# Performance work log

Hardware: AMD Instinct MI355X
Metric: run time of the kernel (lower is better)

The kernel has to match this reference:

```python
import jax, jax.numpy as jnp
import numpy as np

EMBED = 2048
HEADS = 16
NOPE = 128      # embed // heads
VDIM = 128
ROPE = 64
Q_HEAD = NOPE + ROPE  # 192
KV_RANK = 512
BASE = 10000.0


def _rope(x, offset=0):
    # x: [b, h, n, d] with d even; rotary (lrpe_type=1) on pair-interleaved dims
    d = x.shape[-1]
    n = x.shape[-2]
    theta = BASE ** (-2.0 * jnp.arange(d // 2, dtype=jnp.float32) / d)  # [d/2]
    pos = jnp.arange(n, dtype=jnp.float32) + offset                     # [n]
    ang = pos[:, None] * theta[None, :]                                  # [n, d/2]
    cos, sin = jnp.cos(ang), jnp.sin(ang)
    x1 = x[..., 0::2]
    x2 = x[..., 1::2]
    o1 = x1 * cos - x2 * sin
    o2 = x1 * sin + x2 * cos
    return jnp.stack([o1, o2], axis=-1).reshape(x.shape)


def setup_inputs() -> dict:
    key = jax.random.key(0)
    ks = jax.random.split(key, 6)
    b, n = 2, 2048
    s = lambda fin: 1.0 / np.sqrt(fin)
    return {
        "x": jax.random.normal(ks[0], (b, n, EMBED), jnp.float32),
        "Wqa": jax.random.normal(ks[1], (EMBED, 512), jnp.float32) * s(EMBED),
        "Wqb": jax.random.normal(ks[2], (512, HEADS * Q_HEAD), jnp.float32) * s(512),
        "Wkva": jax.random.normal(ks[3], (EMBED, KV_RANK + ROPE), jnp.float32) * s(EMBED),
        "Wkvb": jax.random.normal(ks[4], (KV_RANK, HEADS * (NOPE + VDIM)), jnp.float32) * s(KV_RANK),
        "Wout": jax.random.normal(ks[5], (HEADS * VDIM, EMBED), jnp.float32) * s(HEADS * VDIM),
    }


def reference(x, Wqa, Wqb, Wkva, Wkvb, Wout):
    b, n, _ = x.shape
    # low-rank Q projection
    q = (x @ Wqa) @ Wqb                                   # [b, n, h*192]
    q = q.reshape(b, n, HEADS, Q_HEAD).transpose(0, 2, 1, 3)  # [b, h, n, 192]
    q_nope, q_pe = q[..., :NOPE], q[..., NOPE:]
    # low-rank KV compression + shared rope key
    ckv = x @ Wkva                                        # [b, n, 512+64]
    compressed, k_pe = ckv[..., :KV_RANK], ckv[..., KV_RANK:]
    k_pe = jnp.broadcast_to(k_pe[:, None], (b, HEADS, n, ROPE))
    kv = compressed @ Wkvb                                # [b, n, h*(128+128)]
    kv = kv.reshape(b, n, HEADS, NOPE + VDIM).transpose(0, 2, 1, 3)
    k_nope, v = kv[..., :NOPE], kv[..., NOPE:]
    # partial RoPE on rope slice
    q_pe = _rope(q_pe)
    k_pe = _rope(k_pe)
    qf = jnp.concatenate([q_nope, q_pe], axis=-1)         # [b, h, n, 192]
    kf = jnp.concatenate([k_nope, k_pe], axis=-1)
    # causal SDPA, scale = 1/sqrt(q_head_dim)
    scale = 1.0 / np.sqrt(Q_HEAD)
    scores = jnp.einsum("bhnd,bhmd->bhnm", qf, kf) * scale
    causal = jnp.tril(jnp.ones((n, n), dtype=bool))
    scores = jnp.where(causal, scores, jnp.finfo(scores.dtype).min)
    attn = jax.nn.softmax(scores, axis=-1)
    out = jnp.einsum("bhnm,bhmd->bhnd", attn, v)          # [b, h, n, 128]
    out = out.transpose(0, 2, 1, 3).reshape(b, n, HEADS * VDIM)
    return out @ Wout
```

## Files before the change

### kernel.cpp

```cpp
#include <hip/hip_runtime.h>
#include <math.h>

typedef __bf16 bf16;
typedef __bf16 bf16x8 __attribute__((ext_vector_type(8)));
typedef float f32x4 __attribute__((ext_vector_type(4)));

#define HEADS 16
#define QHEAD 192
#define NB 2
#define SEQ 2048
#define ROWS (NB * SEQ)
#define QSCALE2 0.10411754584f
#define CSHIFT 11.5415603272f

__global__ __launch_bounds__(256) void prep(
    const float* __restrict__ x,
    const float* __restrict__ Wqa, const float* __restrict__ Wqb,
    const float* __restrict__ Wkva, const float* __restrict__ Wkvb,
    const float* __restrict__ Wout,
    bf16* __restrict__ xb,
    bf16* __restrict__ WfT, bf16* __restrict__ WqbT,
    bf16* __restrict__ WkvbT, bf16* __restrict__ WoutT)
{
    int t = blockIdx.x;
    if (t < 8192) {
        size_t i = ((size_t)t * 256 + threadIdx.x) * 4;
        float4 v = *(const float4*)(x + i);
        xb[i]     = (bf16)v.x;
        xb[i + 1] = (bf16)v.y;
        xb[i + 2] = (bf16)v.z;
        xb[i + 3] = (bf16)v.w;
        return;
    }
    t -= 8192;
    __shared__ float tile[32][33];
    const float* in; bf16* out; int R, C;
    if (t < 1024)      {            in = Wqa;  out = WfT;                      R = 2048; C = 512;  }
    else if (t < 2176) { t -= 1024; in = Wkva; out = WfT + (size_t)512 * 2048; R = 2048; C = 576;  }
    else if (t < 3712) { t -= 2176; in = Wqb;  out = WqbT;                     R = 512;  C = 3072; }
    else if (t < 5760) { t -= 3712; in = Wkvb; out = WkvbT;                    R = 512;  C = 4096; }
    else               { t -= 5760; in = Wout; out = WoutT;                    R = 2048; C = 2048; }
    int tilesX = (C + 31) >> 5;
    int bx = (t % tilesX) * 32, by = (t / tilesX) * 32;
    int tx = threadIdx.x & 31, ty = threadIdx.x >> 5;
    for (int i = 0; i < 32; i += 8) {
        int r = by + ty + i, c = bx + tx;
        tile[ty + i][tx] = (r < R && c < C) ? in[(size_t)r * C + c] : 0.f;
    }
    __syncthreads();
    for (int i = 0; i < 32; i += 8) {
        int c = bx + ty + i, r = by + tx;
        if (c < C && r < R) out[(size_t)c * R + r] = (bf16)tile[tx][ty + i];
    }
}

#define GEMM_BODY(Aptr, LDA, Bptr, LDB, KK, BNIDX)                              \
    __shared__ bf16 As[128 * 32];                                               \
    __shared__ bf16 Bs[128 * 32];                                               \
    const int tid  = threadIdx.x;                                               \
    const int wave = tid >> 6, lane = tid & 63;                                 \
    const int quad = lane >> 4, l16 = lane & 15;                                \
    const int bm = blockIdx.x * 128, bn = (BNIDX) * 128;                        \
    const int wm = (wave >> 1) * 64, wn = (wave & 1) * 64;                      \
    const int srow = lane >> 2, scol = (lane & 3) * 8;                          \
    f32x4 acc[4][4];                                                            \
    for (int i = 0; i < 4; i++)                                                 \
        for (int j = 0; j < 4; j++)                                             \
            acc[i][j] = (f32x4){0.f, 0.f, 0.f, 0.f};                            \
    for (int k0 = 0; k0 < (KK); k0 += 32) {                                     \
        _Pragma("unroll")                                                       \
        for (int s2 = 0; s2 < 2; s2++) {                                        \
            const int seg = wave * 2 + s2;                                      \
            const bf16* ga = (Aptr) + (size_t)(bm + seg * 16 + srow) * (LDA) + k0 + scol; \
            const bf16* gb = (Bptr) + (size_t)(bn + seg * 16 + srow) * (LDB) + k0 + scol; \
            __builtin_amdgcn_global_load_lds(                                   \
                (const __attribute__((address_space(1))) void*)ga,              \
                (__attribute__((address_space(3))) void*)&As[seg * 512], 16, 0, 0); \
            __builtin_amdgcn_global_load_lds(                                   \
                (const __attribute__((address_space(1))) void*)gb,              \
                (__attribute__((address_space(3))) void*)&Bs[seg * 512], 16, 0, 0); \
        }                                                                       \
        __syncthreads();                                                        \
        bf16x8 af[4], bfv[4];                                                   \
        for (int mi = 0; mi < 4; mi++)                                          \
            af[mi] = *(const bf16x8*)&As[(wm + mi * 16 + l16) * 32 + quad * 8]; \
        for (int ni = 0; ni < 4; ni++)                                          \
            bfv[ni] = *(const bf16x8*)&Bs[(wn + ni * 16 + l16) * 32 + quad * 8];\
        for (int mi = 0; mi < 4; mi++)                                          \
            for (int ni = 0; ni < 4; ni++)                                      \
                acc[mi][ni] = __builtin_amdgcn_mfma_f32_16x16x32_bf16(          \
                    af[mi], bfv[ni], acc[mi][ni], 0, 0, 0);                     \
        __syncthreads();                                                        \
    }

template <typename OutT>
__global__ __launch_bounds__(256) void gemm_bf16(
    const bf16* __restrict__ A, int lda,
    const bf16* __restrict__ Bt, int ldb,
    OutT* __restrict__ C, int ldc,
    int N, int K)
{
    GEMM_BODY(A, lda, Bt, ldb, K, blockIdx.y)
    for (int mi = 0; mi < 4; mi++)
        for (int ni = 0; ni < 4; ni++) {
            int col = bn + wn + ni * 16 + l16;
            if (col >= N) continue;
            int row0 = bm + wm + mi * 16 + quad * 4;
            for (int r = 0; r < 4; r++)
                C[(size_t)(row0 + r) * ldc + col] = (OutT)acc[mi][ni][r];
        }
}

__global__ __launch_bounds__(256) void gemm_qkv(
    const bf16* __restrict__ tc,
    const bf16* __restrict__ WqbT, const bf16* __restrict__ WkvbT,
    bf16* __restrict__ qf, bf16* __restrict__ kf, bf16* __restrict__ kvv)
{
    const int byAll = blockIdx.y;
    const bool isQ = byAll < 24;
    const bf16* A  = isQ ? tc : tc + 512;
    const bf16* Bt = isQ ? WqbT : WkvbT;
    const int bnIdx = isQ ? byAll : byAll - 24;
    GEMM_BODY(A, 1152, Bt, 512, 512, bnIdx)
    if (isQ) {
        const bool odd = l16 & 1;
        for (int mi = 0; mi < 4; mi++)
            for (int ni = 0; ni < 4; ni++) {
                int col0 = bn + wn + ni * 16;
                int h  = col0 / 192;
                int d0 = col0 - h * 192;
                int d  = d0 + l16;
                bool roped = d0 >= 128;
                float theta = 0.f;
                if (roped) theta = powf(10000.f, -(float)((d - 128) >> 1) / 32.f);
                for (int r = 0; r < 4; r++) {
                    int row = bm + wm + mi * 16 + quad * 4 + r;
                    int b = row >> 11, n = row & 2047;
                    float v = acc[mi][ni][r], res;
                    if (roped) {
                        float p = __shfl_xor(v, 1);
                        float sn, cs;
                        sincosf((float)n * theta, &sn, &cs);
                        float x1 = odd ? p : v, x2 = odd ? v : p;
                        res = odd ? (x1 * sn + x2 * cs) : (x1 * cs - x2 * sn);
                    } else res = v;
                    qf[(((size_t)(b * HEADS + h)) * SEQ + n) * QHEAD + d] =
                        (bf16)(res * QSCALE2);
                }
            }
    } else {
        for (int mi = 0; mi < 4; mi++)
            for (int ni = 0; ni < 4; ni++) {
                int col0 = bn + wn + ni * 16;
                int h  = col0 >> 8;
                int d0 = col0 & 255;
                int d  = d0 + l16;
                for (int r = 0; r < 4; r++) {
                    int row = bm + wm + mi * 16 + quad * 4 + r;
                    int b = row >> 11, n = row & 2047;
                    bf16 v = (bf16)acc[mi][ni][r];
                    if (d0 < 128)
                        kf[(((size_t)(b * HEADS + h)) * SEQ + n) * QHEAD + d] = v;
                    else
                        kvv[(size_t)row * 2048 + h * 128 + (d - 128)] = v;
                }
            }
    }
}

__global__ __launch_bounds__(256) void rope_vt(
    const bf16* __restrict__ tc, const bf16* __restrict__ kvv,
    bf16* __restrict__ kf, bf16* __restrict__ vT)
{
    int t = blockIdx.x;
    if (t < 8192) {
        __shared__ bf16 tile[32][33];
        int bh = t >> 8, rest = t & 255;
        int dv0 = (rest >> 6) * 32, nt0 = (rest & 63) * 32;
        int b = bh >> 4, h = bh & 15;
        int tx = threadIdx.x & 31, ty = threadIdx.x >> 5;
        for (int i = 0; i < 32; i += 8) {
            int n = nt0 + ty + i;
            tile[ty + i][tx] = kvv[((size_t)(b * SEQ + n)) * 2048 + h * 128 + dv0 + tx];
        }
        __syncthreads();
        for (int i = 0; i < 32; i += 8) {
            int dv = dv0 + ty + i;
            vT[((size_t)bh * 128 + dv) * SEQ + nt0 + tx] = tile[tx][ty + i];
        }
    } else {
        int gid = (t - 8192) * 256 + threadIdx.x;
        int row = gid >> 6, j = gid & 63;
        int b = row >> 11, n = row & 2047;
        int i = j >> 1;
        float x1 = (float)tc[(size_t)row * 1152 + 1024 + 2 * i];
        float x2 = (float)tc[(size_t)row * 1152 + 1024 + 2 * i + 1];
        float theta = powf(10000.f, -(float)i / 32.f);
        float sn, cs;
        sincosf((float)n * theta, &sn, &cs);
        bf16 rv = (bf16)((j & 1) ? (x1 * sn + x2 * cs) : (x1 * cs - x2 * sn));
        for (int h = 0; h < HEADS; h++)
            kf[(((size_t)(b * HEADS + h)) * SEQ + n) * QHEAD + 128 + j] = rv;
    }
}

__global__ __launch_bounds__(256) void attn_fa(
    const bf16* __restrict__ qf, const bf16* __restrict__ kf,
    const bf16* __restrict__ vT, bf16* __restrict__ attn_out)
{
    __shared__ bf16 Ks[64][200];
    __shared__ bf16 Vt[128][72];
    __shared__ bf16 Ps[4][16][72];

    const int bid = blockIdx.x;
    const int xcd = bid & 7, j = bid >> 3;
    const int qt = 31 - (j >> 2);
    const int bh = xcd + 8 * (j & 3);
    const int b = bh >> 4, h = bh & 15;
    const int tid  = threadIdx.x;
    const int wave = tid >> 6, lane = tid & 63;
    const int quad = lane >> 4, l16 = lane & 15;

    bf16x8 aq[6];
    {
        const bf16* qbase = qf + ((size_t)bh * SEQ + qt * 64 + wave * 16 + l16) * QHEAD;
        for (int ks = 0; ks < 6; ks++)
            aq[ks] = *(const bf16x8*)(qbase + ks * 32 + quad * 8);
    }
    f32x4 o[8];
    for (int i = 0; i < 8; i++) o[i] = (f32x4){0.f, 0.f, 0.f, 0.f};
    float lp[4] = {0.f, 0.f, 0.f, 0.f};

    for (int kt = 0; kt <= qt; kt++) {
#pragma unroll
        for (int i = 0; i < 6; i++) {
            int c = tid + i * 256;
            int r = c / 24, col = (c - r * 24) * 8;
            *(uint4*)&Ks[r][col] =
                *(const uint4*)(kf + ((size_t)bh * SEQ + kt * 64 + r) * QHEAD + col);
        }
#pragma unroll
        for (int i = 0; i < 4; i++) {
            int c = tid + i * 256;
            int dv = c >> 3, g = c & 7;
            *(uint4*)&Vt[dv][g * 8] =
                *(const uint4*)(vT + ((size_t)bh * 128 + dv) * SEQ + kt * 64 + g * 8);
        }
        __syncthreads();

        f32x4 sacc[4];
        for (int nt = 0; nt < 4; nt++) sacc[nt] = (f32x4){0.f, 0.f, 0.f, 0.f};
        for (int ks = 0; ks < 6; ks++)
            for (int nt = 0; nt < 4; nt++) {
                bf16x8 bk = *(const bf16x8*)&Ks[nt * 16 + l16][ks * 32 + quad * 8];
                sacc[nt] = __builtin_amdgcn_mfma_f32_16x16x32_bf16(aq[ks], bk, sacc[nt], 0, 0, 0);
            }

        const bool diag = (kt == qt);
#pragma unroll
        for (int r = 0; r < 4; r++) {
            const int qrow = wave * 16 + quad * 4 + r;
#pragma unroll
            for (int nt = 0; nt < 4; nt++) {
                float p;
                if (diag && (nt * 16 + l16 > qrow)) p = 0.f;
                else p = __builtin_amdgcn_exp2f(sacc[nt][r] - CSHIFT);
                lp[r] += p;
                Ps[wave][quad * 4 + r][nt * 16 + l16] = (bf16)p;
            }
        }
        __builtin_amdgcn_sched_barrier(0);

        for (int ks2 = 0; ks2 < 2; ks2++) {
            bf16x8 ap = *(const bf16x8*)&Ps[wave][l16][ks2 * 32 + quad * 8];
            for (int nv = 0; nv < 8; nv++) {
                bf16x8 bv = *(const bf16x8*)&Vt[nv * 16 + l16][ks2 * 32 + quad * 8];
                o[nv] = __builtin_amdgcn_mfma_f32_16x16x32_bf16(ap, bv, o[nv], 0, 0, 0);
            }
        }
        __syncthreads();
    }

#pragma unroll
    for (int r = 0; r < 4; r++) {
        lp[r] += __shfl_xor(lp[r], 8);
        lp[r] += __shfl_xor(lp[r], 4);
        lp[r] += __shfl_xor(lp[r], 2);
        lp[r] += __shfl_xor(lp[r], 1);
    }

    for (int r = 0; r < 4; r++) {
        float inv = 1.f / lp[r];
        size_t row = (size_t)b * SEQ + qt * 64 + wave * 16 + quad * 4 + r;
        for (int nv = 0; nv < 8; nv++)
            attn_out[row * 2048 + h * 128 + nv * 16 + l16] = (bf16)(o[nv][r] * inv);
    }
}

extern "C" void kernel_launch(void* const* d_in, const int* in_sizes, int n_in,
                              void* d_out, int out_size, void* d_ws, size_t ws_size,
                              hipStream_t stream)
{
    const float* x    = (const float*)d_in[0];
    const float* Wqa  = (const float*)d_in[1];
    const float* Wqb  = (const float*)d_in[2];
    const float* Wkva = (const float*)d_in[3];
    const float* Wkvb = (const float*)d_in[4];
    const float* Wout = (const float*)d_in[5];
    float* out = (float*)d_out;

    char* ws = (char*)d_ws;
    size_t off = 0;
    auto alloc = [&](size_t elems) { char* p = ws + off; off += elems * sizeof(bf16); return (bf16*)p; };
    bf16* xb    = alloc((size_t)ROWS * 2048);
    bf16* WfT   = alloc((size_t)1152 * 2048);
    bf16* WqbT  = alloc((size_t)3072 * 512);
    bf16* WkvbT = alloc((size_t)4096 * 512);
    bf16* WoutT = alloc((size_t)2048 * 2048);
    bf16* tc    = alloc((size_t)ROWS * 1152);
    bf16* kvv   = alloc((size_t)ROWS * 2048);
    bf16* vT    = alloc((size_t)32 * 128 * SEQ);
    bf16* qf    = alloc((size_t)32 * SEQ * QHEAD);
    bf16* kf    = alloc((size_t)32 * SEQ * QHEAD);
    bf16* attn  = xb;
    if (off > ws_size) return;

    dim3 blk(256);

    prep<<<dim3(18048), blk, 0, stream>>>(x, Wqa, Wqb, Wkva, Wkvb, Wout,
                                          xb, WfT, WqbT, WkvbT, WoutT);

    gemm_bf16<bf16><<<dim3(32, 9), blk, 0, stream>>>(xb, 2048, WfT, 2048, tc, 1152, 1088, 2048);

    gemm_qkv<<<dim3(32, 56), blk, 0, stream>>>(tc, WqbT, WkvbT, qf, kf, kvv);

    rope_vt<<<dim3(9216), blk, 0, stream>>>(tc, kvv, kf, vT);

    attn_fa<<<dim3(1024), blk, 0, stream>>>(qf, kf, vT, attn);

    gemm_bf16<float><<<dim3(32, 16), blk, 0, stream>>>(attn, 2048, WoutT, 2048, out, 2048, 2048, 2048);
}
```

Before: 414.5 us.

## Prefetch next K/V tile into registers and raise MFMA wave priority

The attention kernel now loads the next K and V tiles from global memory into registers while the current tile is being computed, then stores them to shared memory at the start of the next iteration. The aim is to overlap global memory latency with the MFMA work. Address math is precomputed as pointers that advance each iteration, s_setprio raises wave priority around the MFMA loops, and launch bounds now request 2 blocks per SM. The register prefetch buffers add register pressure that could hurt occupancy or cause spills.

```diff
diff --git a/kernel.cpp b/kernel.cpp
--- a/kernel.cpp
+++ b/kernel.cpp
@@ -204,7 +204,7 @@
     }
 }
 
-__global__ __launch_bounds__(256) void attn_fa(
+__global__ __launch_bounds__(256, 2) void attn_fa(
     const bf16* __restrict__ qf, const bf16* __restrict__ kf,
     const bf16* __restrict__ vT, bf16* __restrict__ attn_out)
 {
@@ -231,30 +231,59 @@
     for (int i = 0; i < 8; i++) o[i] = (f32x4){0.f, 0.f, 0.f, 0.f};
     float lp[4] = {0.f, 0.f, 0.f, 0.f};
 
+    const bf16* kp[6]; bf16* ksd[6];
+    const bf16* vp[4]; bf16* vtd[4];
+#pragma unroll
+    for (int i = 0; i < 6; i++) {
+        int c = tid + i * 256;
+        int r = c / 24, col = (c - r * 24) * 8;
+        kp[i]  = kf + ((size_t)bh * SEQ + r) * QHEAD + col;
+        ksd[i] = &Ks[r][col];
+    }
+#pragma unroll
+    for (int i = 0; i < 4; i++) {
+        int c = tid + i * 256;
+        int dv = c >> 3, g = c & 7;
+        vp[i]  = vT + ((size_t)bh * 128 + dv) * SEQ + g * 8;
+        vtd[i] = &Vt[dv][g * 8];
+    }
+
+    uint4 kbuf[6], vbuf[4];
+#pragma unroll
+    for (int i = 0; i < 6; i++) kbuf[i] = *(const uint4*)kp[i];
+#pragma unroll
+    for (int i = 0; i < 4; i++) vbuf[i] = *(const uint4*)vp[i];
+
     for (int kt = 0; kt <= qt; kt++) {
-#pragma unroll
-        for (int i = 0; i < 6; i++) {
-            int c = tid + i * 256;
-            int r = c / 24, col = (c - r * 24) * 8;
-            *(uint4*)&Ks[r][col] =
-                *(const uint4*)(kf + ((size_t)bh * SEQ + kt * 64 + r) * QHEAD + col);
-        }
-#pragma unroll
-        for (int i = 0; i < 4; i++) {
-            int c = tid + i * 256;
-            int dv = c >> 3, g = c & 7;
-            *(uint4*)&Vt[dv][g * 8] =
-                *(const uint4*)(vT + ((size_t)bh * 128 + dv) * SEQ + kt * 64 + g * 8);
-        }
         __syncthreads();
+#pragma unroll
+        for (int i = 0; i < 6; i++) *(uint4*)ksd[i] = kbuf[i];
+#pragma unroll
+        for (int i = 0; i < 4; i++) *(uint4*)vtd[i] = vbuf[i];
+        __syncthreads();
+
+        if (kt < qt) {
+#pragma unroll
+            for (int i = 0; i < 6; i++) {
+                kp[i] += 64 * QHEAD;
+                kbuf[i] = *(const uint4*)kp[i];
+            }
+#pragma unroll
+            for (int i = 0; i < 4; i++) {
+                vp[i] += 64;
+                vbuf[i] = *(const uint4*)vp[i];
+            }
+        }
 
         f32x4 sacc[4];
         for (int nt = 0; nt < 4; nt++) sacc[nt] = (f32x4){0.f, 0.f, 0.f, 0.f};
+        __builtin_amdgcn_s_setprio(1);
         for (int ks = 0; ks < 6; ks++)
             for (int nt = 0; nt < 4; nt++) {
                 bf16x8 bk = *(const bf16x8*)&Ks[nt * 16 + l16][ks * 32 + quad * 8];
                 sacc[nt] = __builtin_amdgcn_mfma_f32_16x16x32_bf16(aq[ks], bk, sacc[nt], 0, 0, 0);
             }
+        __builtin_amdgcn_s_setprio(0);
 
         const bool diag = (kt == qt);
 #pragma unroll
@@ -271,6 +300,7 @@
         }
         __builtin_amdgcn_sched_barrier(0);
 
+        __builtin_amdgcn_s_setprio(1);
         for (int ks2 = 0; ks2 < 2; ks2++) {
             bf16x8 ap = *(const bf16x8*)&Ps[wave][l16][ks2 * 32 + quad * 8];
             for (int nv = 0; nv < 8; nv++) {
@@ -278,7 +308,7 @@
                 o[nv] = __builtin_amdgcn_mfma_f32_16x16x32_bf16(ap, bv, o[nv], 0, 0, 0);
             }
         }
-        __syncthreads();
+        __builtin_amdgcn_s_setprio(0);
     }
 
 #pragma unroll
```

Result: slower. 538.7 us (+30.0%).

## Register-prefetch next K/V tile in attention loop and raise MFMA wave priority

Applied to the files above, without the earlier changes.

The attention kernel now loads the next K and V tile from global memory into registers while the current tile's MFMAs run, and writes them to shared memory at the start of the next iteration. This is meant to hide global load latency behind compute. The barrier structure is reordered, s_setprio raises wave priority around the MFMA blocks, and launch bounds request two blocks per CU. The cost is ten extra uint4 registers per thread, which adds register pressure and could cause spills under the occupancy bound.

```diff
diff --git a/kernel.cpp b/kernel.cpp
--- a/kernel.cpp
+++ b/kernel.cpp
@@ -204,7 +204,7 @@
     }
 }
 
-__global__ __launch_bounds__(256) void attn_fa(
+__global__ __launch_bounds__(256, 2) void attn_fa(
     const bf16* __restrict__ qf, const bf16* __restrict__ kf,
     const bf16* __restrict__ vT, bf16* __restrict__ attn_out)
 {
@@ -231,30 +231,59 @@
     for (int i = 0; i < 8; i++) o[i] = (f32x4){0.f, 0.f, 0.f, 0.f};
     float lp[4] = {0.f, 0.f, 0.f, 0.f};
 
+    const bf16 *kp0, *kp1, *kp2, *kp3, *kp4, *kp5;
+    bf16 *kd0, *kd1, *kd2, *kd3, *kd4, *kd5;
+    const bf16 *vp0, *vp1, *vp2, *vp3;
+    bf16 *vd0, *vd1, *vd2, *vd3;
+#define KINIT(I)                                                                \
+    { int c = tid + I * 256; int r = c / 24, col = (c - r * 24) * 8;            \
+      kp##I = kf + ((size_t)bh * SEQ + r) * QHEAD + col;                        \
+      kd##I = &Ks[r][col]; }
+#define VINIT(I)                                                                \
+    { int c = tid + I * 256; int dv = c >> 3, g = c & 7;                        \
+      vp##I = vT + ((size_t)bh * 128 + dv) * SEQ + g * 8;                       \
+      vd##I = &Vt[dv][g * 8]; }
+    KINIT(0) KINIT(1) KINIT(2) KINIT(3) KINIT(4) KINIT(5)
+    VINIT(0) VINIT(1) VINIT(2) VINIT(3)
+#undef KINIT
+#undef VINIT
+
+    uint4 kb0 = *(const uint4*)kp0, kb1 = *(const uint4*)kp1,
+          kb2 = *(const uint4*)kp2, kb3 = *(const uint4*)kp3,
+          kb4 = *(const uint4*)kp4, kb5 = *(const uint4*)kp5;
+    uint4 vb0 = *(const uint4*)vp0, vb1 = *(const uint4*)vp1,
+          vb2 = *(const uint4*)vp2, vb3 = *(const uint4*)vp3;
+
     for (int kt = 0; kt <= qt; kt++) {
-#pragma unroll
-        for (int i = 0; i < 6; i++) {
-            int c = tid + i * 256;
-            int r = c / 24, col = (c - r * 24) * 8;
-            *(uint4*)&Ks[r][col] =
-                *(const uint4*)(kf + ((size_t)bh * SEQ + kt * 64 + r) * QHEAD + col);
-        }
-#pragma unroll
-        for (int i = 0; i < 4; i++) {
-            int c = tid + i * 256;
-            int dv = c >> 3, g = c & 7;
-            *(uint4*)&Vt[dv][g * 8] =
-                *(const uint4*)(vT + ((size_t)bh * 128 + dv) * SEQ + kt * 64 + g * 8);
-        }
         __syncthreads();
+        *(uint4*)kd0 = kb0; *(uint4*)kd1 = kb1; *(uint4*)kd2 = kb2;
+        *(uint4*)kd3 = kb3; *(uint4*)kd4 = kb4; *(uint4*)kd5 = kb5;
+        *(uint4*)vd0 = vb0; *(uint4*)vd1 = vb1;
+        *(uint4*)vd2 = vb2; *(uint4*)vd3 = vb3;
+        __syncthreads();
+
+        if (kt < qt) {
+            kp0 += 64 * QHEAD; kb0 = *(const uint4*)kp0;
+            kp1 += 64 * QHEAD; kb1 = *(const uint4*)kp1;
+            kp2 += 64 * QHEAD; kb2 = *(const uint4*)kp2;
+            kp3 += 64 * QHEAD; kb3 = *(const uint4*)kp3;
+            kp4 += 64 * QHEAD; kb4 = *(const uint4*)kp4;
+            kp5 += 64 * QHEAD; kb5 = *(const uint4*)kp5;
+            vp0 += 64; vb0 = *(const uint4*)vp0;
+            vp1 += 64; vb1 = *(const uint4*)vp1;
+            vp2 += 64; vb2 = *(const uint4*)vp2;
+            vp3 += 64; vb3 = *(const uint4*)vp3;
+        }
 
         f32x4 sacc[4];
         for (int nt = 0; nt < 4; nt++) sacc[nt] = (f32x4){0.f, 0.f, 0.f, 0.f};
+        __builtin_amdgcn_s_setprio(1);
         for (int ks = 0; ks < 6; ks++)
             for (int nt = 0; nt < 4; nt++) {
                 bf16x8 bk = *(const bf16x8*)&Ks[nt * 16 + l16][ks * 32 + quad * 8];
                 sacc[nt] = __builtin_amdgcn_mfma_f32_16x16x32_bf16(aq[ks], bk, sacc[nt], 0, 0, 0);
             }
+        __builtin_amdgcn_s_setprio(0);
 
         const bool diag = (kt == qt);
 #pragma unroll
@@ -271,6 +300,7 @@
         }
         __builtin_amdgcn_sched_barrier(0);
 
+        __builtin_amdgcn_s_setprio(1);
         for (int ks2 = 0; ks2 < 2; ks2++) {
             bf16x8 ap = *(const bf16x8*)&Ps[wave][l16][ks2 * 32 + quad * 8];
             for (int nv = 0; nv < 8; nv++) {
@@ -278,7 +308,7 @@
                 o[nv] = __builtin_amdgcn_mfma_f32_16x16x32_bf16(ap, bv, o[nv], 0, 0, 0);
             }
         }
-        __syncthreads();
+        __builtin_amdgcn_s_setprio(0);
     }
 
 #pragma unroll
```

New measurement: 407.6 us. About the same (-1.7%).
